# Performance work log

Hardware: AMD Instinct MI355X
Metric: run time of the kernel (lower is better)

Reference implementation:

```python
import jax, jax.numpy as jnp
import numpy as np

B = 2048        # patients (segments)
K = 4           # images per patient
C = 1280        # backbone_out (tf_efficientnet_b0)
PAIRS = K * (K - 1) // 2  # torch.combinations -> 6
NCLS = 1
N_DROP = 5


def setup_inputs() -> dict:
    key = jax.random.key(0)
    ks = jax.random.split(key, 8)
    x = jax.random.normal(ks[0], (B * K, C), jnp.float32)  # detached backbone features
    ids2 = jnp.repeat(jnp.arange(B, dtype=jnp.int32), PAIRS)  # segment id per pair
    Wc = jax.random.normal(ks[1], (C, C, 2), jnp.float32) * 0.02  # Conv1d(C,C,k=2) weight
    bc = jnp.zeros((C,), jnp.float32)
    W0 = jax.random.normal(ks[2], (NCLS, C), jnp.float32) * 0.02
    b0 = jnp.zeros((NCLS,), jnp.float32)
    W1 = jax.random.normal(ks[3], (1, C), jnp.float32) * 0.02
    b1 = jnp.zeros((1,), jnp.float32)
    W2 = jax.random.normal(ks[4], (1, C), jnp.float32) * 0.02
    b2 = jnp.zeros((1,), jnp.float32)
    return dict(x=x, ids2=ids2, Wc=Wc, bc=bc, W0=W0, b0=b0, W1=W1, b1=b1, W2=W2, b2=b2)


def reference(x, ids2, Wc, bc, W0, b0, W1, b1, W2, b2):
    # --- pair combinations within each patient group of K images ---
    ii, jj = np.triu_indices(K, 1)               # static [PAIRS]
    xg = x.reshape(B, K, C)
    xa = xg[:, ii].reshape(B * PAIRS, C)         # first element of each pair
    xb = xg[:, jj].reshape(B * PAIRS, C)         # second element
    # Conv1d(C, C, kernel=2) over the length-2 pair sequence + ReLU
    xc = jax.nn.relu(xa @ Wc[:, :, 0].T + xb @ Wc[:, :, 1].T + bc)  # [P, C]

    # --- 5 fixed dropout masks (p=0.5, train-mode scaling) ---
    masks = jax.random.bernoulli(jax.random.key(42), 0.5,
                                 (N_DROP, xc.shape[0], C)).astype(xc.dtype) * 2.0
    xd = xc[None] * masks                        # [D, P, C]

    cnt = jax.ops.segment_sum(jnp.ones_like(ids2, dtype=xc.dtype),
                              ids2, num_segments=B)  # [B], == PAIRS

    def agg(W, b):
        # head -> scalar mean over classes -> segment-mean over pairs -> mean over dropouts
        z = (jnp.einsum('dpc,oc->dpo', xd, W) + b).mean(-1)          # [D, P]
        s = jax.vmap(lambda u: jax.ops.segment_sum(u, ids2, num_segments=B))(z)
        return (s / cnt).mean(0)                                      # [B]

    logits = agg(W0, b0)
    logits1 = agg(W1, b1)
    logits2 = agg(W2, b2)
    return jnp.stack([logits, logits1, logits2], axis=1)  # [B, 3]
```

## Files before the change

kernel.cpp:

```cpp
#include <hip/hip_runtime.h>


typedef __attribute__((ext_vector_type(8))) short short8;
typedef __attribute__((ext_vector_type(4))) float f32x4;

#define PLANE 15728640u
#define KS2   (0x1BD11BDAu ^ 42u)

__device__ __forceinline__ unsigned short f2bf(float f) {
  unsigned int u = __builtin_bit_cast(unsigned int, f);
  u = (u + 0x7FFFu + ((u >> 16) & 1u)) >> 16;
  return (unsigned short)u;
}
__device__ __forceinline__ float bf2f(unsigned short h) {
  unsigned int u = ((unsigned int)h) << 16;
  return __builtin_bit_cast(float, u);
}

__global__ __launch_bounds__(256) void prep(
    const float* __restrict__ x, unsigned short* __restrict__ xb,
    const float* __restrict__ Wc, unsigned short* __restrict__ Wb) {
  const int bid = blockIdx.x;
  const int t = threadIdx.x;
  if (bid < 2560) {
#pragma unroll
    for (int p = 0; p < 4; p++) {
      const int i4 = bid * 1024 + p * 256 + t;
      const float4 v = ((const float4*)x)[i4];
      ushort4 o;
      o.x = f2bf(v.x); o.y = f2bf(v.y); o.z = f2bf(v.z); o.w = f2bf(v.w);
      ((ushort4*)xb)[i4] = o;
    }
  } else {
    const int i = (bid - 2560) * 256 + t;
    const int n = i / 640;
    const int cin = (i - n * 640) * 2;
    const float4 v = *(const float4*)(Wc + n * 2560 + cin * 2);
    *(ushort2*)(Wb + n * 2560 + cin) =
        make_ushort2(f2bf(v.x), f2bf(v.z));
    *(ushort2*)(Wb + n * 2560 + 1280 + cin) =
        make_ushort2(f2bf(v.y), f2bf(v.w));
  }
}

__device__ __forceinline__ unsigned int rotl(unsigned int x, int r) {
  return __builtin_amdgcn_alignbit(x, x, 32 - r);
}
__device__ __forceinline__ unsigned int tf_msb(unsigned int c) {
  unsigned int x0 = c;
  unsigned int x1 = rotl(c, 13) ^ c;
  x0 += x1; x1 = rotl(x1, 15) ^ x0;
  x0 += x1; x1 = rotl(x1, 26) ^ x0;
  x0 += x1; x1 = rotl(x1, 6)  ^ x0;
  unsigned int t;
  t = x1 + (KS2 + 1u); x0 = x0 + t + 42u; x1 = rotl(t, 17) ^ x0;
  x0 += x1; x1 = rotl(x1, 29) ^ x0;
  x0 += x1; x1 = rotl(x1, 16) ^ x0;
  x0 += x1; x1 = rotl(x1, 24) ^ x0;
  t = x1 + 2u; x0 = x0 + t + KS2; x1 = rotl(t, 13) ^ x0;
  x0 += x1; x1 = rotl(x1, 15) ^ x0;
  x0 += x1; x1 = rotl(x1, 26) ^ x0;
  x0 += x1; x1 = rotl(x1, 6)  ^ x0;
  t = x1 + 45u; x0 = x0 + t; x1 = rotl(t, 17) ^ x0;
  x0 += x1; x1 = rotl(x1, 29) ^ x0;
  x0 += x1; x1 = rotl(x1, 16) ^ x0;
  x0 += x1; x1 = rotl(x1, 24) ^ x0;
  t = x1 + (KS2 + 4u); x0 = x0 + t + 42u; x1 = rotl(t, 13) ^ x0;
  x0 += x1; x1 = rotl(x1, 15) ^ x0;
  x0 += x1; x1 = rotl(x1, 26) ^ x0;
  x0 += x1; x1 = rotl(x1, 6)  ^ x0;
  return ((x0 + KS2) ^ (x1 + 5u)) >> 31;
}

#define GL_LDS(g, l) __builtin_amdgcn_global_load_lds( \
    (const __attribute__((address_space(1))) unsigned int*)(g), \
    (__attribute__((address_space(3))) unsigned int*)(l), 16, 0, 0)

__global__ __launch_bounds__(256) void mixed(
    const unsigned short* __restrict__ Xb,
    const unsigned short* __restrict__ Wb,
    unsigned short* __restrict__ U0b,
    unsigned short* __restrict__ U1b,
    unsigned int* __restrict__ Spk)
{
  __shared__ unsigned short sA[128 * 32];
  __shared__ unsigned short sB[128 * 32];
  const int bid = blockIdx.x;
  const int t = threadIdx.x;

  if (bid < 512) {
    const int D0 = bid * 3840 + t;
    for (int g = 0; g < 15; ++g) {
      const int D = D0 + g * 256;
      const unsigned int bg = (unsigned int)D * 8u + 42u;
      unsigned int zacc = 0;
#pragma unroll
      for (int sub = 0; sub < 8; ++sub) {
        const unsigned int b = bg + (unsigned int)sub;
        const unsigned int z5 = tf_msb(b) + tf_msb(b + PLANE) +
                                tf_msb(b + 2u * PLANE) + tf_msb(b + 3u * PLANE) +
                                tf_msb(b + 4u * PLANE);
        zacc |= z5 << (4 * sub);
      }
      Spk[D] = zacc;
    }
    return;
  }

  const int id = bid - 512;
  const int xcd = id & 7;
  const int slot = id >> 3;
  const int mband = xcd * 8 + slot / 20;
  const int nst = slot % 20;
  const int side = nst / 10;
  const int n0 = (nst % 10) * 128;
  const int p0 = mband * 128;

  const int lane = t & 63, w = t >> 6;
  const int wr = w >> 1, wc = w & 1;
  const int mrow = lane & 15;
  const int koff = (lane >> 4) * 8;
  const int srow = lane >> 2, schk = (lane & 3) * 8;

  unsigned short* const ldsA0 = sA + (w * 32 + 0) * 32;
  unsigned short* const ldsA1 = sA + (w * 32 + 16) * 32;
  unsigned short* const ldsB0 = sB + (w * 32 + 0) * 32;
  unsigned short* const ldsB1 = sB + (w * 32 + 16) * 32;
  const unsigned short* const gA0 = Xb + (p0 + w * 32 + srow) * 1280 + schk;
  const unsigned short* const gA1 = Xb + (p0 + w * 32 + 16 + srow) * 1280 + schk;
  const unsigned short* const gB0 =
      Wb + (n0 + w * 32 + srow) * 2560 + side * 1280 + schk;
  const unsigned short* const gB1 =
      Wb + (n0 + w * 32 + 16 + srow) * 2560 + side * 1280 + schk;

  f32x4 acc[4][4];
#pragma unroll
  for (int i = 0; i < 4; i++)
#pragma unroll
    for (int j = 0; j < 4; j++) acc[i][j] = (f32x4){0.f, 0.f, 0.f, 0.f};

  for (int k0 = 0; k0 < 1280; k0 += 32) {
    __syncthreads();
    GL_LDS(gA0 + k0, ldsA0);
    GL_LDS(gA1 + k0, ldsA1);
    GL_LDS(gB0 + k0, ldsB0);
    GL_LDS(gB1 + k0, ldsB1);
    __syncthreads();
    short8 af[4], bfr[4];
#pragma unroll
    for (int i = 0; i < 4; i++)
      af[i] = *(const short8*)(sA + (wr * 64 + i * 16 + mrow) * 32 + koff);
#pragma unroll
    for (int j = 0; j < 4; j++)
      bfr[j] = *(const short8*)(sB + (wc * 64 + j * 16 + mrow) * 32 + koff);
#pragma unroll
    for (int i = 0; i < 4; i++)
#pragma unroll
      for (int j = 0; j < 4; j++)
        acc[i][j] = __builtin_amdgcn_mfma_f32_16x16x32_bf16(af[i], bfr[j],
                                                            acc[i][j], 0, 0, 0);
  }

  unsigned short* const U = side ? U1b : U0b;
  const int mq = (lane >> 4) * 4;
  const int nn = lane & 15;
#pragma unroll
  for (int j = 0; j < 4; j++) {
    const int n = n0 + wc * 64 + j * 16 + nn;
#pragma unroll
    for (int i = 0; i < 4; i++) {
      const int prow = p0 + wr * 64 + i * 16 + mq;
#pragma unroll
      for (int rg = 0; rg < 4; rg++)
        U[(prow + rg) * 1280 + n] = f2bf(acc[i][j][rg]);
    }
  }
}

__global__ __launch_bounds__(256) void combine(
    const unsigned short* __restrict__ U0b, const unsigned short* __restrict__ U1b,
    const unsigned int* __restrict__ Spk, const float* __restrict__ bc,
    const float* __restrict__ W0, const float* __restrict__ W1,
    const float* __restrict__ W2,
    const float* __restrict__ b0, const float* __restrict__ b1,
    const float* __restrict__ b2, float* __restrict__ out)
{
  const int pat = blockIdx.x;
  const int t = threadIdx.x;
  const int rbase = pat * 4 * 1280;
  const int sbase = pat * 6 * 160;
  float s0 = 0.f, s1 = 0.f, s2 = 0.f;

  for (int qi = 0; qi < 5; qi++) {
    const int c = qi * 256 + t;
    const float w0 = W0[c], w1 = W1[c], w2 = W2[c], bcv = bc[c];
    const float u00 = bf2f(U0b[rbase + c]);
    const float u01 = bf2f(U0b[rbase + 1280 + c]);
    const float u02 = bf2f(U0b[rbase + 2560 + c]);
    const float u11 = bf2f(U1b[rbase + 1280 + c]);
    const float u12 = bf2f(U1b[rbase + 2560 + c]);
    const float u13 = bf2f(U1b[rbase + 3840 + c]);
    const float pv[6] = {u00 + u11, u00 + u12, u00 + u13,
                         u01 + u12, u01 + u13, u02 + u13};
    const int cd = c >> 3, cn = 4 * (c & 7);
#pragma unroll
    for (int pr = 0; pr < 6; pr++) {
      float v = pv[pr] + bcv;
      v = v > 0.f ? v : 0.f;
      const int z = (int)((Spk[sbase + pr * 160 + cd] >> cn) & 7u);
      const float tx = v * (float)(5 - z);
      s0 += tx * w0; s1 += tx * w1; s2 += tx * w2;
    }
  }

#pragma unroll
  for (int off = 32; off > 0; off >>= 1) {
    s0 += __shfl_xor(s0, off); s1 += __shfl_xor(s1, off); s2 += __shfl_xor(s2, off);
  }
  __shared__ float red[4][3];
  const int lane = t & 63, w = t >> 6;
  if (lane == 0) { red[w][0] = s0; red[w][1] = s1; red[w][2] = s2; }
  __syncthreads();
  if (t == 0) {
    const float r0 = red[0][0] + red[1][0] + red[2][0] + red[3][0];
    const float r1 = red[0][1] + red[1][1] + red[2][1] + red[3][1];
    const float r2 = red[0][2] + red[1][2] + red[2][2] + red[3][2];
    out[pat * 3 + 0] = b0[0] + r0 * (1.0f / 15.0f);
    out[pat * 3 + 1] = b1[0] + r1 * (1.0f / 15.0f);
    out[pat * 3 + 2] = b2[0] + r2 * (1.0f / 15.0f);
  }
}

extern "C" void kernel_launch(void* const* d_in, const int* in_sizes, int n_in,
                              void* d_out, int out_size, void* d_ws, size_t ws_size,
                              hipStream_t stream) {
  const float* x  = (const float*)d_in[0];
  const float* Wc = (const float*)d_in[2];
  const float* bc = (const float*)d_in[3];
  const float* W0 = (const float*)d_in[4];
  const float* b0 = (const float*)d_in[5];
  const float* W1 = (const float*)d_in[6];
  const float* b1 = (const float*)d_in[7];
  const float* W2 = (const float*)d_in[8];
  const float* b2 = (const float*)d_in[9];
  float* out = (float*)d_out;

  char* ws = (char*)d_ws;
  unsigned short* xb  = (unsigned short*)ws;
  unsigned short* Wb  = (unsigned short*)(ws + 20971520);
  unsigned short* U0b = (unsigned short*)(ws + 27525120);
  unsigned short* U1b = (unsigned short*)(ws + 48496640);
  unsigned int*   Spk = (unsigned int*)(ws + 69468160);

  prep<<<5760, 256, 0, stream>>>(x, xb, Wc, Wb);
  mixed<<<1792, 256, 0, stream>>>(xb, Wb, U0b, U1b, Spk);
  combine<<<2048, 256, 0, stream>>>(U0b, U1b, Spk, bc, W0, W1, W2,
                                    b0, b1, b2, out);
}
```

Measured before the change: 295.0 us.

## Interleave dropout-mask RNG generation into GEMM K-loop of every block

Removes the 512 dedicated Threefry mask-generation blocks and instead has each of the 1280 GEMM blocks compute a slice of the packed dropout-mask counts inside its K-loop, between issuing the async global-to-LDS loads and the barrier. The RNG is batched as six independent Threefry streams per call to expose ILP. The aim is to hide the integer ALU work under load latency and MFMA execution, and to shrink the grid. The cost is higher register pressure in the GEMM kernel, which could reduce occupancy or delay the MFMA issue.

Result: faster. 279.0 us (-5.5%).

```diff
diff --git a/kernel.cpp b/kernel.cpp
--- a/kernel.cpp
+++ b/kernel.cpp
@@ -46,30 +46,55 @@
 __device__ __forceinline__ unsigned int rotl(unsigned int x, int r) {
   return __builtin_amdgcn_alignbit(x, x, 32 - r);
 }
-__device__ __forceinline__ unsigned int tf_msb(unsigned int c) {
-  unsigned int x0 = c;
-  unsigned int x1 = rotl(c, 13) ^ c;
-  x0 += x1; x1 = rotl(x1, 15) ^ x0;
-  x0 += x1; x1 = rotl(x1, 26) ^ x0;
-  x0 += x1; x1 = rotl(x1, 6)  ^ x0;
-  unsigned int t;
-  t = x1 + (KS2 + 1u); x0 = x0 + t + 42u; x1 = rotl(t, 17) ^ x0;
-  x0 += x1; x1 = rotl(x1, 29) ^ x0;
-  x0 += x1; x1 = rotl(x1, 16) ^ x0;
-  x0 += x1; x1 = rotl(x1, 24) ^ x0;
-  t = x1 + 2u; x0 = x0 + t + KS2; x1 = rotl(t, 13) ^ x0;
-  x0 += x1; x1 = rotl(x1, 15) ^ x0;
-  x0 += x1; x1 = rotl(x1, 26) ^ x0;
-  x0 += x1; x1 = rotl(x1, 6)  ^ x0;
-  t = x1 + 45u; x0 = x0 + t; x1 = rotl(t, 17) ^ x0;
-  x0 += x1; x1 = rotl(x1, 29) ^ x0;
-  x0 += x1; x1 = rotl(x1, 16) ^ x0;
-  x0 += x1; x1 = rotl(x1, 24) ^ x0;
-  t = x1 + (KS2 + 4u); x0 = x0 + t + 42u; x1 = rotl(t, 13) ^ x0;
-  x0 += x1; x1 = rotl(x1, 15) ^ x0;
-  x0 += x1; x1 = rotl(x1, 26) ^ x0;
-  x0 += x1; x1 = rotl(x1, 6)  ^ x0;
-  return ((x0 + KS2) ^ (x1 + 5u)) >> 31;
+
+__device__ __forceinline__ unsigned int tf_msb6(const unsigned int cbase) {
+  unsigned int x0[6], x1[6];
+#pragma unroll
+  for (int q = 0; q < 6; q++) {
+    const unsigned int c = cbase + (unsigned int)q * 2048u;
+    x0[q] = c;
+    x1[q] = rotl(c, 13) ^ c;
+  }
+#define R6(r)                                                   \
+  _Pragma("unroll") for (int q = 0; q < 6; q++) {               \
+    x0[q] += x1[q];                                             \
+    x1[q] = rotl(x1[q], (r)) ^ x0[q];                           \
+  }
+  R6(15) R6(26) R6(6)
+#pragma unroll
+  for (int q = 0; q < 6; q++) {
+    const unsigned int u = x1[q] + (KS2 + 1u);
+    x0[q] = x0[q] + u + 42u;
+    x1[q] = rotl(u, 17) ^ x0[q];
+  }
+  R6(29) R6(16) R6(24)
+#pragma unroll
+  for (int q = 0; q < 6; q++) {
+    const unsigned int u = x1[q] + 2u;
+    x0[q] = x0[q] + u + KS2;
+    x1[q] = rotl(u, 13) ^ x0[q];
+  }
+  R6(15) R6(26) R6(6)
+#pragma unroll
+  for (int q = 0; q < 6; q++) {
+    const unsigned int u = x1[q] + 45u;
+    x0[q] = x0[q] + u;
+    x1[q] = rotl(u, 17) ^ x0[q];
+  }
+  R6(29) R6(16) R6(24)
+#pragma unroll
+  for (int q = 0; q < 6; q++) {
+    const unsigned int u = x1[q] + (KS2 + 4u);
+    x0[q] = x0[q] + u + 42u;
+    x1[q] = rotl(u, 13) ^ x0[q];
+  }
+  R6(15) R6(26) R6(6)
+#undef R6
+  unsigned int bits = 0;
+#pragma unroll
+  for (int q = 0; q < 6; q++)
+    bits |= (((x0[q] + KS2) ^ (x1[q] + 5u)) >> 31) << q;
+  return bits;
 }
 
 #define GL_LDS(g, l) __builtin_amdgcn_global_load_lds( \
@@ -88,26 +113,7 @@
   const int bid = blockIdx.x;
   const int t = threadIdx.x;
 
-  if (bid < 512) {
-    const int D0 = bid * 3840 + t;
-    for (int g = 0; g < 15; ++g) {
-      const int D = D0 + g * 256;
-      const unsigned int bg = (unsigned int)D * 8u + 42u;
-      unsigned int zacc = 0;
-#pragma unroll
-      for (int sub = 0; sub < 8; ++sub) {
-        const unsigned int b = bg + (unsigned int)sub;
-        const unsigned int z5 = tf_msb(b) + tf_msb(b + PLANE) +
-                                tf_msb(b + 2u * PLANE) + tf_msb(b + 3u * PLANE) +
-                                tf_msb(b + 4u * PLANE);
-        zacc |= z5 << (4 * sub);
-      }
-      Spk[D] = zacc;
-    }
-    return;
-  }
-
-  const int id = bid - 512;
+  const int id = bid;
   const int xcd = id & 7;
   const int slot = id >> 3;
   const int mband = xcd * 8 + slot / 20;
@@ -139,12 +145,25 @@
 #pragma unroll
     for (int j = 0; j < 4; j++) acc[i][j] = (f32x4){0.f, 0.f, 0.f, 0.f};
 
+  unsigned int zacc[6] = {0u, 0u, 0u, 0u, 0u, 0u};
+  const unsigned int c8 = ((unsigned int)bid * 1536u + (unsigned int)t) * 8u;
+
   for (int k0 = 0; k0 < 1280; k0 += 32) {
     __syncthreads();
     GL_LDS(gA0 + k0, ldsA0);
     GL_LDS(gA1 + k0, ldsA1);
     GL_LDS(gB0 + k0, ldsB0);
     GL_LDS(gB1 + k0, ldsB1);
+    {
+      const int ks = k0 >> 5;
+      const int sub = ks & 7;
+      const int dpl = ks >> 3;
+      const unsigned int bits =
+          tf_msb6(c8 + (unsigned int)sub + 42u + (unsigned int)dpl * PLANE);
+#pragma unroll
+      for (int q = 0; q < 6; q++)
+        zacc[q] += ((bits >> q) & 1u) << (4 * sub);
+    }
     __syncthreads();
     short8 af[4], bfr[4];
 #pragma unroll
@@ -160,6 +179,10 @@
         acc[i][j] = __builtin_amdgcn_mfma_f32_16x16x32_bf16(af[i], bfr[j],
                                                             acc[i][j], 0, 0, 0);
   }
+
+#pragma unroll
+  for (int q = 0; q < 6; q++)
+    Spk[bid * 1536 + q * 256 + t] = zacc[q];
 
   unsigned short* const U = side ? U1b : U0b;
   const int mq = (lane >> 4) * 4;
@@ -253,7 +276,7 @@
   unsigned int*   Spk = (unsigned int*)(ws + 69468160);
 
   prep<<<5760, 256, 0, stream>>>(x, xb, Wc, Wb);
-  mixed<<<1792, 256, 0, stream>>>(xb, Wb, U0b, U1b, Spk);
+  mixed<<<1280, 256, 0, stream>>>(xb, Wb, U0b, U1b, Spk);
   combine<<<2048, 256, 0, stream>>>(U0b, U1b, Spk, bc, W0, W1, W2,
                                     b0, b1, b2, out);
 }
```
